# Optimization experiments

Measured on AMD Instinct MI355X. Metric: run time of the kernel, lower is better.

Reference implementation:

```python
import jax, jax.numpy as jnp
import numpy as np

B, S, T, C, H = 16, 64, 4096, 512, 8
D = C // H
NEG = jnp.float32(-1e30)


def setup_inputs() -> dict:
    key = jax.random.key(0)
    ks = jax.random.split(key, 12)
    x = jax.random.normal(ks[0], (1, C, 1), dtype=jnp.float32)
    eh = jax.random.normal(ks[1], (B, C, T), dtype=jnp.float32)
    # ragged shot boundaries -> fixed (B, S) start/end arrays, end > start
    bounds = jnp.sort(jax.random.randint(ks[2], (B, S + 1), 0, T), axis=-1)
    shot_starts = bounds[:, :-1].astype(jnp.int32)
    shot_ends = jnp.maximum(bounds[:, 1:], shot_starts + 1).astype(jnp.int32)
    sc = 1.0 / np.sqrt(C)
    Wq = jax.random.normal(ks[3], (C, C), dtype=jnp.float32) * sc
    bq = jnp.zeros((C,), dtype=jnp.float32)
    Wk = jax.random.normal(ks[4], (C, C), dtype=jnp.float32) * sc
    bk = jnp.zeros((C,), dtype=jnp.float32)
    Wv = jax.random.normal(ks[5], (C, C), dtype=jnp.float32) * sc
    bv = jnp.zeros((C,), dtype=jnp.float32)
    Wp = jax.random.normal(ks[6], (C, C), dtype=jnp.float32) * sc
    bp = jnp.zeros((C,), dtype=jnp.float32)
    return {"x": x, "encoder_hidden_states": eh, "shot_starts": shot_starts,
            "shot_ends": shot_ends, "Wq": Wq, "bq": bq, "Wk": Wk, "bk": bk,
            "Wv": Wv, "bv": bv, "Wp": Wp, "bp": bp}


def reference(x, encoder_hidden_states, shot_starts, shot_ends,
              Wq, bq, Wk, bk, Wv, bv, Wp, bp):
    scale = 1.0 / np.sqrt(D)
    # 1x1 conv == pointwise matmul over channels
    q = (Wq @ x[0] + bq[:, None])            # (C, 1)
    k = jnp.einsum('oc,bct->bot', Wk, encoder_hidden_states) + bk[None, :, None]
    v = jnp.einsum('oc,bct->bot', Wv, encoder_hidden_states) + bv[None, :, None]
    qh = q.reshape(H, D) * scale             # (H, D) single query per head
    kh = k.reshape(B, H, D, T)               # (B, H, D, T)
    vh = v.reshape(B, H, D, T).transpose(0, 1, 3, 2)  # (B, H, T, D)
    att = jnp.einsum('hd,bhdt->bht', qh, kh)          # (B, H, T)
    pos = jnp.arange(T)
    seg = (pos[None, None, :] >= shot_starts[:, :, None]) & \
          (pos[None, None, :] < shot_ends[:, :, None])  # (B, S, T)
    logits = jnp.where(seg[:, :, None, :], att[:, None, :, :], NEG)  # (B,S,H,T)
    p = jax.nn.softmax(logits, axis=-1)
    out = jnp.einsum('bsht,bhtd->bshd', p, vh)        # (B, S, H, D)
    out = out.reshape(B * S, C)
    out = out @ Wp.T + bp                              # proj (1x1 conv)
    return out[:, :, None]                             # (B*S, C, 1)
```

## Files before the change

kernel.cpp:

```cpp
#include <hip/hip_runtime.h>
#include <cstdint>
#include <cstddef>

#define B_ 16
#define S_ 64
#define T_ 4096
#define C_ 512
#define H_ 8

#define WS_QKT     0
#define WS_QB      4096
#define WS_QH      4104
#define WS_MS      4616
#define WS_LI      12808
#define WS_CNT     21000
#define WS_CSEG    21016
#define WS_CIDX    23064
#define WS_CMUL    25112
#define WS_ATT     28672
#define WS_WSUM    552960
#define WS_ATTNOUT 4747264

__global__ void k_prep1(const float* __restrict__ x, const float* __restrict__ Wq,
                        const float* __restrict__ bq, float* __restrict__ qh_g) {
  __shared__ float xs[C_];
  __shared__ float red[256];
  int tid = threadIdx.x;
  xs[tid] = x[tid];
  xs[tid + 256] = x[tid + 256];
  __syncthreads();
  int r0 = blockIdx.x * 32;
  int rl = tid >> 3, sub = tid & 7;
  int r = r0 + rl;
  const float* wr = Wq + (size_t)r * C_ + sub * 64;
  const float* xp = xs + sub * 64;
  float s = 0.f;
#pragma unroll
  for (int i = 0; i < 64; i += 4) {
    float4 w = *(const float4*)(wr + i);
    s += w.x * xp[i] + w.y * xp[i + 1] + w.z * xp[i + 2] + w.w * xp[i + 3];
  }
  red[tid] = s;
  __syncthreads();
  if (sub == 0) {
    float tot = bq[r];
#pragma unroll
    for (int i = 0; i < 8; ++i) tot += red[rl * 8 + i];
    qh_g[r] = tot * 0.125f;
  }
}

__global__ void k_prep2(const float* __restrict__ qh_g,
                        const float* __restrict__ Wk,
                        const float* __restrict__ bk, float* __restrict__ qkT,
                        float* __restrict__ qb) {
  __shared__ float qhs[64];
  int tid = threadIdx.x;
  int h = blockIdx.x;
  if (tid < 64) qhs[tid] = qh_g[h * 64 + tid];
  __syncthreads();
  int c0 = tid, c1 = tid + 256;
  float s0 = 0.f, s1 = 0.f;
#pragma unroll 8
  for (int d = 0; d < 64; ++d) {
    const float* row = Wk + (size_t)(h * 64 + d) * C_;
    float q = qhs[d];
    s0 += q * row[c0];
    s1 += q * row[c1];
  }
  qkT[c0 * 8 + h] = s0;
  qkT[c1 * 8 + h] = s1;
  if (tid < 64) {
    float w = qhs[tid] * bk[h * 64 + tid];
#pragma unroll
    for (int off = 32; off > 0; off >>= 1) w += __shfl_down(w, off, 64);
    if (tid == 0) qb[h] = w;
  }
}

__global__ __launch_bounds__(256, 4) void k_att(
    const float* __restrict__ eh, const float* __restrict__ qkT,
    const float* __restrict__ qb, float* __restrict__ att) {
  __shared__ float qks[C_ * 8];
  __shared__ float part[4 * 8 * 64];
  int tid = threadIdx.x;
  int tl = tid & 63, cg = tid >> 6;
  int b = blockIdx.y;
  int t0 = blockIdx.x * 64;
#pragma unroll
  for (int i = 0; i < 16; ++i) qks[tid + i * 256] = qkT[tid + i * 256];
  __syncthreads();
  const float* ehp = eh + ((size_t)b * C_ + (size_t)cg * 128) * T_ + t0 + tl;
  float acc[8];
#pragma unroll
  for (int h = 0; h < 8; ++h) acc[h] = 0.f;
#pragma unroll 4
  for (int j = 0; j < 128; ++j) {
    float e = ehp[(size_t)j * T_];
    const float4 q0 = *(const float4*)&qks[(cg * 128 + j) * 8];
    const float4 q1 = *(const float4*)&qks[(cg * 128 + j) * 8 + 4];
    acc[0] += q0.x * e; acc[1] += q0.y * e; acc[2] += q0.z * e; acc[3] += q0.w * e;
    acc[4] += q1.x * e; acc[5] += q1.y * e; acc[6] += q1.z * e; acc[7] += q1.w * e;
  }
#pragma unroll
  for (int h = 0; h < 8; ++h) part[(cg * 8 + h) * 64 + tl] = acc[h];
  __syncthreads();
#pragma unroll
  for (int i = 0; i < 2; ++i) {
    int idx = tid + i * 256;
    int h = idx >> 6, tt = idx & 63;
    float v = part[(0 * 8 + h) * 64 + tt] + part[(1 * 8 + h) * 64 + tt] +
              part[(2 * 8 + h) * 64 + tt] + part[(3 * 8 + h) * 64 + tt] + qb[h];
    att[((size_t)b * H_ + h) * T_ + t0 + tt] = v;
  }
}

__global__ void k_stats(const float* __restrict__ att,
                        const int* __restrict__ starts,
                        const int* __restrict__ ends, float* __restrict__ ms,
                        float* __restrict__ li) {
  int tid = threadIdx.x;
  int n = blockIdx.x;
  int b = n >> 6;
  int start = starts[n], end = ends[n];
  int h = tid >> 5, tl = tid & 31;
  const float* ah = att + ((size_t)b * H_ + h) * T_;
  float mloc = -3.0e38f;
  for (int t = start + tl; t < end; t += 32) mloc = fmaxf(mloc, ah[t]);
#pragma unroll
  for (int off = 16; off > 0; off >>= 1)
    mloc = fmaxf(mloc, __shfl_xor(mloc, off, 32));
  float lloc = 0.f;
  for (int t = start + tl; t < end; t += 32) lloc += __expf(ah[t] - mloc);
#pragma unroll
  for (int off = 16; off > 0; off >>= 1) lloc += __shfl_xor(lloc, off, 32);
  if (tl == 0) { ms[n * 8 + h] = mloc; li[n * 8 + h] = 1.f / lloc; }
}

__global__ void k_map(const int* __restrict__ starts,
                      const int* __restrict__ ends, int* __restrict__ cnt,
                      int* __restrict__ cseg, int* __restrict__ cidx,
                      int* __restrict__ cmul) {
  __shared__ int sc[1024];
  int n = threadIdx.x;
  int st = starts[n], en = ends[n];
  int cbase = st & ~15;
  int nch = (en - cbase + 127) >> 7;
  sc[n] = nch;
  __syncthreads();
  for (int off = 1; off < 1024; off <<= 1) {
    int v = 0;
    if (n >= off) v = sc[n - off];
    __syncthreads();
    sc[n] += v;
    __syncthreads();
  }
  int pre = sc[n] - nch;
  for (int k = 0; k < nch; ++k) {
    cseg[pre + k] = n;
    cidx[pre + k] = k;
    cmul[pre + k] = (nch > 1) ? 1 : 0;
  }
  if (n == 1023) cnt[0] = sc[n];
}

__global__ __launch_bounds__(256, 4) void k_wsum(
    const float* __restrict__ eh, const float* __restrict__ att,
    const float* __restrict__ ms, const float* __restrict__ li,
    const int* __restrict__ starts, const int* __restrict__ ends,
    const int* __restrict__ cnt, const int* __restrict__ cseg,
    const int* __restrict__ cidx, const int* __restrict__ cmul,
    float* __restrict__ wsum) {
  __shared__ float pl[8 * 136];
  int i = blockIdx.x;
  if (i >= cnt[0]) return;
  int tid = threadIdx.x;
  int n = cseg[i];
  int k = cidx[i];
  int mul = cmul[i];
  int b = n >> 6;
  int st = starts[n], en = ends[n];
  int cbase = st & ~15;
  int base = cbase + (k << 7);
  int t_lo = (st > base) ? st : base;
  int t_hi = base + 128;
  if (en < t_hi) t_hi = en;
  int jmax = t_hi - base;
  int kmax = (jmax + 15) >> 4;

  {
    int h = tid >> 5, l32 = tid & 31;
    float msn = ms[n * 8 + h], lin = li[n * 8 + h];
    const float* ah = att + ((size_t)b * H_ + h) * T_;
    for (int j = l32; j < 136; j += 32) {
      int t = base + j;
      float pv = 0.f;
      if (t >= t_lo && t < t_hi) pv = __expf(ah[t] - msn) * lin;
      pl[h * 136 + j] = pv;
    }
  }
  __syncthreads();

  int l = tid & 63, wv = tid >> 6;
  int il = l & 3, g = l >> 2;
  float* wp = wsum + (size_t)n * (H_ * C_);

  for (int pass = 0; pass < 8; ++pass) {
    int ch = pass * 64 + wv * 16 + g;
    const float* erow = eh + ((size_t)b * C_ + ch) * T_;
    float a0 = 0.f, a1 = 0.f, a2 = 0.f, a3 = 0.f;
    float a4 = 0.f, a5 = 0.f, a6 = 0.f, a7 = 0.f;
#pragma unroll 2
    for (int kk = 0; kk < kmax; ++kk) {
      int j0 = (kk << 4) | (il << 2);
      int tg = base + j0;
      if (tg > T_ - 4) tg = T_ - 4;
      float4 ev = *(const float4*)(erow + tg);
      const float* pp = pl + j0;
      float4 p;
      p = *(const float4*)(pp + 0 * 136);
      a0 += p.x * ev.x + p.y * ev.y + p.z * ev.z + p.w * ev.w;
      p = *(const float4*)(pp + 1 * 136);
      a1 += p.x * ev.x + p.y * ev.y + p.z * ev.z + p.w * ev.w;
      p = *(const float4*)(pp + 2 * 136);
      a2 += p.x * ev.x + p.y * ev.y + p.z * ev.z + p.w * ev.w;
      p = *(const float4*)(pp + 3 * 136);
      a3 += p.x * ev.x + p.y * ev.y + p.z * ev.z + p.w * ev.w;
      p = *(const float4*)(pp + 4 * 136);
      a4 += p.x * ev.x + p.y * ev.y + p.z * ev.z + p.w * ev.w;
      p = *(const float4*)(pp + 5 * 136);
      a5 += p.x * ev.x + p.y * ev.y + p.z * ev.z + p.w * ev.w;
      p = *(const float4*)(pp + 6 * 136);
      a6 += p.x * ev.x + p.y * ev.y + p.z * ev.z + p.w * ev.w;
      p = *(const float4*)(pp + 7 * 136);
      a7 += p.x * ev.x + p.y * ev.y + p.z * ev.z + p.w * ev.w;
    }
    a0 += __shfl_xor(a0, 1); a0 += __shfl_xor(a0, 2);
    a1 += __shfl_xor(a1, 1); a1 += __shfl_xor(a1, 2);
    a2 += __shfl_xor(a2, 1); a2 += __shfl_xor(a2, 2);
    a3 += __shfl_xor(a3, 1); a3 += __shfl_xor(a3, 2);
    a4 += __shfl_xor(a4, 1); a4 += __shfl_xor(a4, 2);
    a5 += __shfl_xor(a5, 1); a5 += __shfl_xor(a5, 2);
    a6 += __shfl_xor(a6, 1); a6 += __shfl_xor(a6, 2);
    a7 += __shfl_xor(a7, 1); a7 += __shfl_xor(a7, 2);
    float s0 = (il < 2) ? ((il == 0) ? a0 : a2) : ((il == 2) ? a4 : a6);
    float s1 = (il < 2) ? ((il == 0) ? a1 : a3) : ((il == 2) ? a5 : a7);
    int h0 = il << 1;
    if (!mul) {
      wp[h0 * C_ + ch] = s0;
      wp[(h0 + 1) * C_ + ch] = s1;
    } else {
      atomicAdd(&wp[h0 * C_ + ch], s0);
      atomicAdd(&wp[(h0 + 1) * C_ + ch], s1);
    }
  }
}

__global__ __launch_bounds__(256, 4) void k_gemm(
    const float* __restrict__ A, long aRow, long aColPerY,
    const float* __restrict__ Bm, const float* __restrict__ bias,
    float* __restrict__ Cc) {
  __shared__ float As[32 * 36];
  __shared__ float Bs[64 * 36];
  int tid = threadIdx.x;
  int n0 = blockIdx.x * 32;
  int y = blockIdx.y;
  const float* Abase = A + (size_t)n0 * aRow + (size_t)y * aColPerY;
  const float* Bbase = Bm + (size_t)(y * 64) * C_;
  int tx = tid & 15, ty = tid >> 4;
  float acc[2][4];
#pragma unroll
  for (int a = 0; a < 2; ++a)
#pragma unroll
    for (int bb = 0; bb < 4; ++bb) acc[a][bb] = 0.f;
  for (int k0 = 0; k0 < 512; k0 += 32) {
#pragma unroll
    for (int i = 0; i < 4; ++i) {
      int idx = tid + i * 256;
      int r = idx >> 5, cc = idx & 31;
      As[r * 36 + cc] = Abase[(size_t)r * aRow + k0 + cc];
    }
#pragma unroll
    for (int i = 0; i < 8; ++i) {
      int idx = tid + i * 256;
      int r = idx >> 5, cc = idx & 31;
      Bs[r * 36 + cc] = Bbase[(size_t)r * C_ + k0 + cc];
    }
    __syncthreads();
#pragma unroll
    for (int k = 0; k < 32; k += 4) {
      const float4 a0 = *(const float4*)&As[(ty * 2 + 0) * 36 + k];
      const float4 a1 = *(const float4*)&As[(ty * 2 + 1) * 36 + k];
#pragma unroll
      for (int bb = 0; bb < 4; ++bb) {
        const float4 bv = *(const float4*)&Bs[(tx * 4 + bb) * 36 + k];
        acc[0][bb] += a0.x * bv.x + a0.y * bv.y + a0.z * bv.z + a0.w * bv.w;
        acc[1][bb] += a1.x * bv.x + a1.y * bv.y + a1.z * bv.z + a1.w * bv.w;
      }
    }
    __syncthreads();
  }
#pragma unroll
  for (int a = 0; a < 2; ++a) {
    int nn = n0 + ty * 2 + a;
    float4 o;
    o.x = acc[a][0] + bias[y * 64 + tx * 4 + 0];
    o.y = acc[a][1] + bias[y * 64 + tx * 4 + 1];
    o.z = acc[a][2] + bias[y * 64 + tx * 4 + 2];
    o.w = acc[a][3] + bias[y * 64 + tx * 4 + 3];
    *(float4*)&Cc[(size_t)nn * C_ + y * 64 + tx * 4] = o;
  }
}

extern "C" void kernel_launch(void* const* d_in, const int* in_sizes, int n_in,
                              void* d_out, int out_size, void* d_ws,
                              size_t ws_size, hipStream_t stream) {
  const float* x = (const float*)d_in[0];
  const float* eh = (const float*)d_in[1];
  const int* shot_starts = (const int*)d_in[2];
  const int* shot_ends = (const int*)d_in[3];
  const float* Wq = (const float*)d_in[4];
  const float* bq = (const float*)d_in[5];
  const float* Wk = (const float*)d_in[6];
  const float* bk = (const float*)d_in[7];
  const float* Wv = (const float*)d_in[8];
  const float* bv = (const float*)d_in[9];
  const float* Wp = (const float*)d_in[10];
  const float* bp = (const float*)d_in[11];
  float* out = (float*)d_out;

  float* ws = (float*)d_ws;
  float* qkT = ws + WS_QKT;
  float* qb = ws + WS_QB;
  float* qh = ws + WS_QH;
  float* ms = ws + WS_MS;
  float* li = ws + WS_LI;
  int* cnt = (int*)(ws + WS_CNT);
  int* cseg = (int*)(ws + WS_CSEG);
  int* cidx = (int*)(ws + WS_CIDX);
  int* cmul = (int*)(ws + WS_CMUL);
  float* att = ws + WS_ATT;
  float* wsum = ws + WS_WSUM;
  float* attnout = ws + WS_ATTNOUT;

  hipMemsetAsync(wsum, 0, (size_t)1024 * H_ * C_ * sizeof(float), stream);
  k_prep1<<<16, 256, 0, stream>>>(x, Wq, bq, qh);
  k_prep2<<<8, 256, 0, stream>>>(qh, Wk, bk, qkT, qb);
  k_att<<<dim3(T_ / 64, B_), 256, 0, stream>>>(eh, qkT, qb, att);
  k_stats<<<B_ * S_, 256, 0, stream>>>(att, shot_starts, shot_ends, ms, li);
  k_map<<<1, 1024, 0, stream>>>(shot_starts, shot_ends, cnt, cseg, cidx, cmul);
  k_wsum<<<2048, 256, 0, stream>>>(eh, att, ms, li, shot_starts, shot_ends,
                                   cnt, cseg, cidx, cmul, wsum);
  k_gemm<<<dim3(32, 8), 256, 0, stream>>>(wsum, (long)(H_ * C_), (long)C_, Wv,
                                          bv, attnout);
  k_gemm<<<dim3(32, 8), 256, 0, stream>>>(attnout, (long)C_, 0L, Wp, bp, out);
}
```

Baseline: 347.4 us.

## Fold chunk mapping into stats kernel and block wsum over four channels

Removes the single-block k_map prefix-scan kernel: the chunk count is zeroed in k_prep1, and each k_stats block claims its chunk-list slots with an atomicAdd. This saves one launch and a serial 1024-thread scan. The order of chunks now depends on scheduling but stays consistent, and writes are clamped to 2048 entries. Separately, k_wsum now computes four channels per thread per pass instead of one, so each LDS probability load is reused across four eh rows, at the cost of 32 accumulators and more register pressure.

```diff
diff --git a/kernel.cpp b/kernel.cpp
--- a/kernel.cpp
+++ b/kernel.cpp
@@ -22,10 +22,12 @@
 #define WS_ATTNOUT 4747264
 
 __global__ void k_prep1(const float* __restrict__ x, const float* __restrict__ Wq,
-                        const float* __restrict__ bq, float* __restrict__ qh_g) {
+                        const float* __restrict__ bq, float* __restrict__ qh_g,
+                        int* __restrict__ cnt) {
   __shared__ float xs[C_];
   __shared__ float red[256];
   int tid = threadIdx.x;
+  if (blockIdx.x == 0 && tid == 0) cnt[0] = 0;
   xs[tid] = x[tid];
   xs[tid + 256] = x[tid + 256];
   __syncthreads();
@@ -118,11 +120,25 @@
 __global__ void k_stats(const float* __restrict__ att,
                         const int* __restrict__ starts,
                         const int* __restrict__ ends, float* __restrict__ ms,
-                        float* __restrict__ li) {
+                        float* __restrict__ li, int* __restrict__ cnt,
+                        int* __restrict__ cseg, int* __restrict__ cidx,
+                        int* __restrict__ cmul) {
   int tid = threadIdx.x;
   int n = blockIdx.x;
   int b = n >> 6;
   int start = starts[n], end = ends[n];
+  if (tid == 0) {
+    int cb = start & ~15;
+    int nch = (end - cb + 127) >> 7;
+    int pre = atomicAdd(cnt, nch);
+    int lim = 2048 - pre;
+    if (nch < lim) lim = nch;
+    for (int k = 0; k < lim; ++k) {
+      cseg[pre + k] = n;
+      cidx[pre + k] = k;
+      cmul[pre + k] = (nch > 1) ? 1 : 0;
+    }
+  }
   int h = tid >> 5, tl = tid & 31;
   const float* ah = att + ((size_t)b * H_ + h) * T_;
   float mloc = -3.0e38f;
@@ -135,33 +151,6 @@
 #pragma unroll
   for (int off = 16; off > 0; off >>= 1) lloc += __shfl_xor(lloc, off, 32);
   if (tl == 0) { ms[n * 8 + h] = mloc; li[n * 8 + h] = 1.f / lloc; }
-}
-
-__global__ void k_map(const int* __restrict__ starts,
-                      const int* __restrict__ ends, int* __restrict__ cnt,
-                      int* __restrict__ cseg, int* __restrict__ cidx,
-                      int* __restrict__ cmul) {
-  __shared__ int sc[1024];
-  int n = threadIdx.x;
-  int st = starts[n], en = ends[n];
-  int cbase = st & ~15;
-  int nch = (en - cbase + 127) >> 7;
-  sc[n] = nch;
-  __syncthreads();
-  for (int off = 1; off < 1024; off <<= 1) {
-    int v = 0;
-    if (n >= off) v = sc[n - off];
-    __syncthreads();
-    sc[n] += v;
-    __syncthreads();
-  }
-  int pre = sc[n] - nch;
-  for (int k = 0; k < nch; ++k) {
-    cseg[pre + k] = n;
-    cidx[pre + k] = k;
-    cmul[pre + k] = (nch > 1) ? 1 : 0;
-  }
-  if (n == 1023) cnt[0] = sc[n];
 }
 
 __global__ __launch_bounds__(256, 4) void k_wsum(
@@ -205,53 +194,58 @@
   int il = l & 3, g = l >> 2;
   float* wp = wsum + (size_t)n * (H_ * C_);
 
-  for (int pass = 0; pass < 8; ++pass) {
-    int ch = pass * 64 + wv * 16 + g;
-    const float* erow = eh + ((size_t)b * C_ + ch) * T_;
-    float a0 = 0.f, a1 = 0.f, a2 = 0.f, a3 = 0.f;
-    float a4 = 0.f, a5 = 0.f, a6 = 0.f, a7 = 0.f;
+#pragma unroll
+  for (int p2 = 0; p2 < 2; ++p2) {
+    int ch0 = p2 * 256 + wv * 64 + g;
+    const float* er0 = eh + ((size_t)b * C_ + ch0) * T_;
+    float acc[4][8];
+#pragma unroll
+    for (int cc = 0; cc < 4; ++cc)
+#pragma unroll
+      for (int h = 0; h < 8; ++h) acc[cc][h] = 0.f;
 #pragma unroll 2
     for (int kk = 0; kk < kmax; ++kk) {
       int j0 = (kk << 4) | (il << 2);
       int tg = base + j0;
       if (tg > T_ - 4) tg = T_ - 4;
-      float4 ev = *(const float4*)(erow + tg);
+      float4 ev[4];
+#pragma unroll
+      for (int cc = 0; cc < 4; ++cc)
+        ev[cc] = *(const float4*)(er0 + (size_t)(cc * 16) * T_ + tg);
       const float* pp = pl + j0;
-      float4 p;
-      p = *(const float4*)(pp + 0 * 136);
-      a0 += p.x * ev.x + p.y * ev.y + p.z * ev.z + p.w * ev.w;
-      p = *(const float4*)(pp + 1 * 136);
-      a1 += p.x * ev.x + p.y * ev.y + p.z * ev.z + p.w * ev.w;
-      p = *(const float4*)(pp + 2 * 136);
-      a2 += p.x * ev.x + p.y * ev.y + p.z * ev.z + p.w * ev.w;
-      p = *(const float4*)(pp + 3 * 136);
-      a3 += p.x * ev.x + p.y * ev.y + p.z * ev.z + p.w * ev.w;
-      p = *(const float4*)(pp + 4 * 136);
-      a4 += p.x * ev.x + p.y * ev.y + p.z * ev.z + p.w * ev.w;
-      p = *(const float4*)(pp + 5 * 136);
-      a5 += p.x * ev.x + p.y * ev.y + p.z * ev.z + p.w * ev.w;
-      p = *(const float4*)(pp + 6 * 136);
-      a6 += p.x * ev.x + p.y * ev.y + p.z * ev.z + p.w * ev.w;
-      p = *(const float4*)(pp + 7 * 136);
-      a7 += p.x * ev.x + p.y * ev.y + p.z * ev.z + p.w * ev.w;
-    }
-    a0 += __shfl_xor(a0, 1); a0 += __shfl_xor(a0, 2);
-    a1 += __shfl_xor(a1, 1); a1 += __shfl_xor(a1, 2);
-    a2 += __shfl_xor(a2, 1); a2 += __shfl_xor(a2, 2);
-    a3 += __shfl_xor(a3, 1); a3 += __shfl_xor(a3, 2);
-    a4 += __shfl_xor(a4, 1); a4 += __shfl_xor(a4, 2);
-    a5 += __shfl_xor(a5, 1); a5 += __shfl_xor(a5, 2);
-    a6 += __shfl_xor(a6, 1); a6 += __shfl_xor(a6, 2);
-    a7 += __shfl_xor(a7, 1); a7 += __shfl_xor(a7, 2);
-    float s0 = (il < 2) ? ((il == 0) ? a0 : a2) : ((il == 2) ? a4 : a6);
-    float s1 = (il < 2) ? ((il == 0) ? a1 : a3) : ((il == 2) ? a5 : a7);
-    int h0 = il << 1;
-    if (!mul) {
-      wp[h0 * C_ + ch] = s0;
-      wp[(h0 + 1) * C_ + ch] = s1;
-    } else {
-      atomicAdd(&wp[h0 * C_ + ch], s0);
-      atomicAdd(&wp[(h0 + 1) * C_ + ch], s1);
+#pragma unroll
+      for (int h = 0; h < 8; ++h) {
+        float4 pf = *(const float4*)(pp + h * 136);
+#pragma unroll
+        for (int cc = 0; cc < 4; ++cc)
+          acc[cc][h] += pf.x * ev[cc].x + pf.y * ev[cc].y +
+                        pf.z * ev[cc].z + pf.w * ev[cc].w;
+      }
+    }
+#pragma unroll
+    for (int cc = 0; cc < 4; ++cc)
+#pragma unroll
+      for (int h = 0; h < 8; ++h) {
+        acc[cc][h] += __shfl_xor(acc[cc][h], 1);
+        acc[cc][h] += __shfl_xor(acc[cc][h], 2);
+      }
+#pragma unroll
+    for (int cc = 0; cc < 4; ++cc) {
+      int ch = ch0 + cc * 16;
+      float s0 = (il == 0) ? acc[cc][0]
+               : (il == 1) ? acc[cc][2]
+               : (il == 2) ? acc[cc][4] : acc[cc][6];
+      float s1 = (il == 0) ? acc[cc][1]
+               : (il == 1) ? acc[cc][3]
+               : (il == 2) ? acc[cc][5] : acc[cc][7];
+      int h0 = il << 1;
+      if (!mul) {
+        wp[h0 * C_ + ch] = s0;
+        wp[(h0 + 1) * C_ + ch] = s1;
+      } else {
+        atomicAdd(&wp[h0 * C_ + ch], s0);
+        atomicAdd(&wp[(h0 + 1) * C_ + ch], s1);
+      }
     }
   }
 }
@@ -344,11 +338,11 @@
   float* attnout = ws + WS_ATTNOUT;
 
   hipMemsetAsync(wsum, 0, (size_t)1024 * H_ * C_ * sizeof(float), stream);
-  k_prep1<<<16, 256, 0, stream>>>(x, Wq, bq, qh);
+  k_prep1<<<16, 256, 0, stream>>>(x, Wq, bq, qh, cnt);
   k_prep2<<<8, 256, 0, stream>>>(qh, Wk, bk, qkT, qb);
   k_att<<<dim3(T_ / 64, B_), 256, 0, stream>>>(eh, qkT, qb, att);
-  k_stats<<<B_ * S_, 256, 0, stream>>>(att, shot_starts, shot_ends, ms, li);
-  k_map<<<1, 1024, 0, stream>>>(shot_starts, shot_ends, cnt, cseg, cidx, cmul);
+  k_stats<<<B_ * S_, 256, 0, stream>>>(att, shot_starts, shot_ends, ms, li,
+                                       cnt, cseg, cidx, cmul);
   k_wsum<<<2048, 256, 0, stream>>>(eh, att, ms, li, shot_starts, shot_ends,
                                    cnt, cseg, cidx, cmul, wsum);
   k_gemm<<<dim3(32, 8), 256, 0, stream>>>(wsum, (long)(H_ * C_), (long)C_, Wv,
```

After: 357.6 us. 2.9% more time.

## Fold chunk map into prep kernel, zero wsum selectively, widen attention tiles

Applied to the files above, without the earlier changes.

Moves the shot-chunk prefix-scan map into an extra block of k_prep1, which removes a separate single-block launch. The full memset of the wsum buffer is replaced by zeroing inside k_stats, and only for segments that span more than one chunk and so accumulate atomically. k_att now has each thread handle four timesteps with float4 loads, giving 256 timesteps per block and a quarter as many blocks. The trade-offs are a larger shared-memory buffer in k_att, fewer blocks to fill the GPU, and a correctness dependence on single-chunk segments writing every element of their wsum rows.

```diff
diff --git a/kernel.cpp b/kernel.cpp
--- a/kernel.cpp
+++ b/kernel.cpp
@@ -22,10 +22,51 @@
 #define WS_ATTNOUT 4747264
 
 __global__ void k_prep1(const float* __restrict__ x, const float* __restrict__ Wq,
-                        const float* __restrict__ bq, float* __restrict__ qh_g) {
+                        const float* __restrict__ bq, float* __restrict__ qh_g,
+                        const int* __restrict__ starts,
+                        const int* __restrict__ ends, int* __restrict__ cnt,
+                        int* __restrict__ cseg, int* __restrict__ cidx,
+                        int* __restrict__ cmul) {
   __shared__ float xs[C_];
   __shared__ float red[256];
-  int tid = threadIdx.x;
+  __shared__ int sc2[256];
+  int tid = threadIdx.x;
+  if (blockIdx.x == 16) {
+    int n0 = tid * 4;
+    int st0 = starts[n0 + 0], en0 = ends[n0 + 0];
+    int st1 = starts[n0 + 1], en1 = ends[n0 + 1];
+    int st2 = starts[n0 + 2], en2 = ends[n0 + 2];
+    int st3 = starts[n0 + 3], en3 = ends[n0 + 3];
+    int c0 = (en0 - (st0 & ~15) + 127) >> 7;
+    int c1 = (en1 - (st1 & ~15) + 127) >> 7;
+    int c2 = (en2 - (st2 & ~15) + 127) >> 7;
+    int c3 = (en3 - (st3 & ~15) + 127) >> 7;
+    int loc = c0 + c1 + c2 + c3;
+    sc2[tid] = loc;
+    __syncthreads();
+    for (int off = 1; off < 256; off <<= 1) {
+      int v = (tid >= off) ? sc2[tid - off] : 0;
+      __syncthreads();
+      sc2[tid] += v;
+      __syncthreads();
+    }
+    int pre = sc2[tid] - loc;
+#define EMIT(cX, nX)                                                  \
+    {                                                                 \
+      int m = (cX > 1) ? 1 : 0;                                       \
+      for (int k = 0; k < cX; ++k) {                                  \
+        cseg[pre + k] = nX; cidx[pre + k] = k; cmul[pre + k] = m;     \
+      }                                                               \
+      pre += cX;                                                      \
+    }
+    EMIT(c0, n0 + 0)
+    EMIT(c1, n0 + 1)
+    EMIT(c2, n0 + 2)
+    EMIT(c3, n0 + 3)
+#undef EMIT
+    if (tid == 255) cnt[0] = sc2[255];
+    return;
+  }
   xs[tid] = x[tid];
   xs[tid + 256] = x[tid + 256];
   __syncthreads();
@@ -82,35 +123,41 @@
     const float* __restrict__ eh, const float* __restrict__ qkT,
     const float* __restrict__ qb, float* __restrict__ att) {
   __shared__ float qks[C_ * 8];
-  __shared__ float part[4 * 8 * 64];
+  __shared__ float part[4 * 8 * 256];
   int tid = threadIdx.x;
   int tl = tid & 63, cg = tid >> 6;
   int b = blockIdx.y;
-  int t0 = blockIdx.x * 64;
+  int t0 = blockIdx.x * 256;
 #pragma unroll
   for (int i = 0; i < 16; ++i) qks[tid + i * 256] = qkT[tid + i * 256];
   __syncthreads();
-  const float* ehp = eh + ((size_t)b * C_ + (size_t)cg * 128) * T_ + t0 + tl;
-  float acc[8];
-#pragma unroll
-  for (int h = 0; h < 8; ++h) acc[h] = 0.f;
+  const float* ehp =
+      eh + ((size_t)b * C_ + (size_t)cg * 128) * T_ + t0 + tl * 4;
+  float4 acc[8];
+#pragma unroll
+  for (int h = 0; h < 8; ++h) acc[h] = make_float4(0.f, 0.f, 0.f, 0.f);
+#define FMA4(A, s)                                                       \
+  A.x += (s)*ev.x; A.y += (s)*ev.y; A.z += (s)*ev.z; A.w += (s)*ev.w;
 #pragma unroll 4
   for (int j = 0; j < 128; ++j) {
-    float e = ehp[(size_t)j * T_];
+    float4 ev = *(const float4*)&ehp[(size_t)j * T_];
     const float4 q0 = *(const float4*)&qks[(cg * 128 + j) * 8];
     const float4 q1 = *(const float4*)&qks[(cg * 128 + j) * 8 + 4];
-    acc[0] += q0.x * e; acc[1] += q0.y * e; acc[2] += q0.z * e; acc[3] += q0.w * e;
-    acc[4] += q1.x * e; acc[5] += q1.y * e; acc[6] += q1.z * e; acc[7] += q1.w * e;
-  }
-#pragma unroll
-  for (int h = 0; h < 8; ++h) part[(cg * 8 + h) * 64 + tl] = acc[h];
-  __syncthreads();
-#pragma unroll
-  for (int i = 0; i < 2; ++i) {
+    FMA4(acc[0], q0.x) FMA4(acc[1], q0.y) FMA4(acc[2], q0.z) FMA4(acc[3], q0.w)
+    FMA4(acc[4], q1.x) FMA4(acc[5], q1.y) FMA4(acc[6], q1.z) FMA4(acc[7], q1.w)
+  }
+#undef FMA4
+#pragma unroll
+  for (int h = 0; h < 8; ++h)
+    *(float4*)&part[(cg * 8 + h) * 256 + tl * 4] = acc[h];
+  __syncthreads();
+#pragma unroll
+  for (int i = 0; i < 8; ++i) {
     int idx = tid + i * 256;
-    int h = idx >> 6, tt = idx & 63;
-    float v = part[(0 * 8 + h) * 64 + tt] + part[(1 * 8 + h) * 64 + tt] +
-              part[(2 * 8 + h) * 64 + tt] + part[(3 * 8 + h) * 64 + tt] + qb[h];
+    int h = idx >> 8, tt = idx & 255;
+    float v = part[(0 * 8 + h) * 256 + tt] + part[(1 * 8 + h) * 256 + tt] +
+              part[(2 * 8 + h) * 256 + tt] + part[(3 * 8 + h) * 256 + tt] +
+              qb[h];
     att[((size_t)b * H_ + h) * T_ + t0 + tt] = v;
   }
 }
@@ -118,11 +165,18 @@
 __global__ void k_stats(const float* __restrict__ att,
                         const int* __restrict__ starts,
                         const int* __restrict__ ends, float* __restrict__ ms,
-                        float* __restrict__ li) {
+                        float* __restrict__ li, float* __restrict__ wsum) {
   int tid = threadIdx.x;
   int n = blockIdx.x;
   int b = n >> 6;
   int start = starts[n], end = ends[n];
+  int nch = (end - (start & ~15) + 127) >> 7;
+  if (nch > 1) {
+    float4 z = make_float4(0.f, 0.f, 0.f, 0.f);
+    float* wrow = wsum + (size_t)n * (H_ * C_);
+#pragma unroll
+    for (int i2 = 0; i2 < 4; ++i2) *(float4*)&wrow[(tid + i2 * 256) * 4] = z;
+  }
   int h = tid >> 5, tl = tid & 31;
   const float* ah = att + ((size_t)b * H_ + h) * T_;
   float mloc = -3.0e38f;
@@ -135,33 +189,6 @@
 #pragma unroll
   for (int off = 16; off > 0; off >>= 1) lloc += __shfl_xor(lloc, off, 32);
   if (tl == 0) { ms[n * 8 + h] = mloc; li[n * 8 + h] = 1.f / lloc; }
-}
-
-__global__ void k_map(const int* __restrict__ starts,
-                      const int* __restrict__ ends, int* __restrict__ cnt,
-                      int* __restrict__ cseg, int* __restrict__ cidx,
-                      int* __restrict__ cmul) {
-  __shared__ int sc[1024];
-  int n = threadIdx.x;
-  int st = starts[n], en = ends[n];
-  int cbase = st & ~15;
-  int nch = (en - cbase + 127) >> 7;
-  sc[n] = nch;
-  __syncthreads();
-  for (int off = 1; off < 1024; off <<= 1) {
-    int v = 0;
-    if (n >= off) v = sc[n - off];
-    __syncthreads();
-    sc[n] += v;
-    __syncthreads();
-  }
-  int pre = sc[n] - nch;
-  for (int k = 0; k < nch; ++k) {
-    cseg[pre + k] = n;
-    cidx[pre + k] = k;
-    cmul[pre + k] = (nch > 1) ? 1 : 0;
-  }
-  if (n == 1023) cnt[0] = sc[n];
 }
 
 __global__ __launch_bounds__(256, 4) void k_wsum(
@@ -343,12 +370,12 @@
   float* wsum = ws + WS_WSUM;
   float* attnout = ws + WS_ATTNOUT;
 
-  hipMemsetAsync(wsum, 0, (size_t)1024 * H_ * C_ * sizeof(float), stream);
-  k_prep1<<<16, 256, 0, stream>>>(x, Wq, bq, qh);
+  k_prep1<<<17, 256, 0, stream>>>(x, Wq, bq, qh, shot_starts, shot_ends, cnt,
+                                  cseg, cidx, cmul);
   k_prep2<<<8, 256, 0, stream>>>(qh, Wk, bk, qkT, qb);
-  k_att<<<dim3(T_ / 64, B_), 256, 0, stream>>>(eh, qkT, qb, att);
-  k_stats<<<B_ * S_, 256, 0, stream>>>(att, shot_starts, shot_ends, ms, li);
-  k_map<<<1, 1024, 0, stream>>>(shot_starts, shot_ends, cnt, cseg, cidx, cmul);
+  k_att<<<dim3(T_ / 256, B_), 256, 0, stream>>>(eh, qkT, qb, att);
+  k_stats<<<B_ * S_, 256, 0, stream>>>(att, shot_starts, shot_ends, ms, li,
+                                       wsum);
   k_wsum<<<2048, 256, 0, stream>>>(eh, att, ms, li, shot_starts, shot_ends,
                                    cnt, cseg, cidx, cmul, wsum);
   k_gemm<<<dim3(32, 8), 256, 0, stream>>>(wsum, (long)(H_ * C_), (long)C_, Wv,
```

Measured after the change: 339.1 us, median of 2. -2.4%, faster.

## Fuse attention logits, segment softmax, and weighted sum into one per-segment kernel

Applied to the files above, without the earlier changes.

Replaces the separate logit, stats, chunk-map and weighted-sum kernels with one kernel that runs one block per shot segment. Each block walks its segment in 64-token chunks: it recomputes the logits from the encoder states, applies an online softmax with running max and sum in shared memory, and accumulates the weighted channel sums in shared memory. This removes the global logit buffer round trip, the memset, the atomics and several launches. The cost is that one block processes a whole segment serially, so long segments cause load imbalance, and the larger shared-memory footprint lowers the occupancy target.

```diff
diff --git a/kernel.cpp b/kernel.cpp
--- a/kernel.cpp
+++ b/kernel.cpp
@@ -11,13 +11,6 @@
 #define WS_QKT     0
 #define WS_QB      4096
 #define WS_QH      4104
-#define WS_MS      4616
-#define WS_LI      12808
-#define WS_CNT     21000
-#define WS_CSEG    21016
-#define WS_CIDX    23064
-#define WS_CMUL    25112
-#define WS_ATT     28672
 #define WS_WSUM    552960
 #define WS_ATTNOUT 4747264
 
@@ -78,181 +71,171 @@
   }
 }
 
-__global__ __launch_bounds__(256, 4) void k_att(
+__global__ __launch_bounds__(256, 3) void k_fused(
     const float* __restrict__ eh, const float* __restrict__ qkT,
-    const float* __restrict__ qb, float* __restrict__ att) {
-  __shared__ float qks[C_ * 8];
-  __shared__ float part[4 * 8 * 64];
-  int tid = threadIdx.x;
-  int tl = tid & 63, cg = tid >> 6;
-  int b = blockIdx.y;
-  int t0 = blockIdx.x * 64;
-#pragma unroll
-  for (int i = 0; i < 16; ++i) qks[tid + i * 256] = qkT[tid + i * 256];
-  __syncthreads();
-  const float* ehp = eh + ((size_t)b * C_ + (size_t)cg * 128) * T_ + t0 + tl;
-  float acc[8];
-#pragma unroll
-  for (int h = 0; h < 8; ++h) acc[h] = 0.f;
-#pragma unroll 4
-  for (int j = 0; j < 128; ++j) {
-    float e = ehp[(size_t)j * T_];
-    const float4 q0 = *(const float4*)&qks[(cg * 128 + j) * 8];
-    const float4 q1 = *(const float4*)&qks[(cg * 128 + j) * 8 + 4];
-    acc[0] += q0.x * e; acc[1] += q0.y * e; acc[2] += q0.z * e; acc[3] += q0.w * e;
-    acc[4] += q1.x * e; acc[5] += q1.y * e; acc[6] += q1.z * e; acc[7] += q1.w * e;
-  }
-#pragma unroll
-  for (int h = 0; h < 8; ++h) part[(cg * 8 + h) * 64 + tl] = acc[h];
-  __syncthreads();
-#pragma unroll
-  for (int i = 0; i < 2; ++i) {
-    int idx = tid + i * 256;
-    int h = idx >> 6, tt = idx & 63;
-    float v = part[(0 * 8 + h) * 64 + tt] + part[(1 * 8 + h) * 64 + tt] +
-              part[(2 * 8 + h) * 64 + tt] + part[(3 * 8 + h) * 64 + tt] + qb[h];
-    att[((size_t)b * H_ + h) * T_ + t0 + tt] = v;
-  }
-}
-
-__global__ void k_stats(const float* __restrict__ att,
-                        const int* __restrict__ starts,
-                        const int* __restrict__ ends, float* __restrict__ ms,
-                        float* __restrict__ li) {
+    const float* __restrict__ qb_g, const int* __restrict__ starts,
+    const int* __restrict__ ends, float* __restrict__ wsum) {
+  __shared__ __attribute__((aligned(16))) float qks[C_ * 8];
+  __shared__ __attribute__((aligned(16))) float part[4 * 8 * 64];
+  __shared__ __attribute__((aligned(16))) float ps[8 * 72];
+  __shared__ __attribute__((aligned(16))) float accw[C_ * 8];
+  __shared__ float qbs[8], mlds[8], llds[8], flds[8];
   int tid = threadIdx.x;
   int n = blockIdx.x;
   int b = n >> 6;
-  int start = starts[n], end = ends[n];
-  int h = tid >> 5, tl = tid & 31;
-  const float* ah = att + ((size_t)b * H_ + h) * T_;
-  float mloc = -3.0e38f;
-  for (int t = start + tl; t < end; t += 32) mloc = fmaxf(mloc, ah[t]);
-#pragma unroll
-  for (int off = 16; off > 0; off >>= 1)
-    mloc = fmaxf(mloc, __shfl_xor(mloc, off, 32));
-  float lloc = 0.f;
-  for (int t = start + tl; t < end; t += 32) lloc += __expf(ah[t] - mloc);
-#pragma unroll
-  for (int off = 16; off > 0; off >>= 1) lloc += __shfl_xor(lloc, off, 32);
-  if (tl == 0) { ms[n * 8 + h] = mloc; li[n * 8 + h] = 1.f / lloc; }
-}
-
-__global__ void k_map(const int* __restrict__ starts,
-                      const int* __restrict__ ends, int* __restrict__ cnt,
-                      int* __restrict__ cseg, int* __restrict__ cidx,
-                      int* __restrict__ cmul) {
-  __shared__ int sc[1024];
-  int n = threadIdx.x;
   int st = starts[n], en = ends[n];
-  int cbase = st & ~15;
-  int nch = (en - cbase + 127) >> 7;
-  sc[n] = nch;
+  int base0 = st & ~15;
+  int nch = (en - base0 + 63) >> 6;
+
+#pragma unroll
+  for (int i2 = 0; i2 < 16; ++i2) qks[tid + i2 * 256] = qkT[tid + i2 * 256];
+#pragma unroll
+  for (int i2 = 0; i2 < 16; ++i2) accw[tid + i2 * 256] = 0.f;
+  if (tid < 8) {
+    qbs[tid] = qb_g[tid];
+    mlds[tid] = -3.0e38f;
+    llds[tid] = 0.f;
+  }
   __syncthreads();
-  for (int off = 1; off < 1024; off <<= 1) {
-    int v = 0;
-    if (n >= off) v = sc[n - off];
-    __syncthreads();
-    sc[n] += v;
-    __syncthreads();
-  }
-  int pre = sc[n] - nch;
-  for (int k = 0; k < nch; ++k) {
-    cseg[pre + k] = n;
-    cidx[pre + k] = k;
-    cmul[pre + k] = (nch > 1) ? 1 : 0;
-  }
-  if (n == 1023) cnt[0] = sc[n];
-}
-
-__global__ __launch_bounds__(256, 4) void k_wsum(
-    const float* __restrict__ eh, const float* __restrict__ att,
-    const float* __restrict__ ms, const float* __restrict__ li,
-    const int* __restrict__ starts, const int* __restrict__ ends,
-    const int* __restrict__ cnt, const int* __restrict__ cseg,
-    const int* __restrict__ cidx, const int* __restrict__ cmul,
-    float* __restrict__ wsum) {
-  __shared__ float pl[8 * 136];
-  int i = blockIdx.x;
-  if (i >= cnt[0]) return;
-  int tid = threadIdx.x;
-  int n = cseg[i];
-  int k = cidx[i];
-  int mul = cmul[i];
-  int b = n >> 6;
-  int st = starts[n], en = ends[n];
-  int cbase = st & ~15;
-  int base = cbase + (k << 7);
-  int t_lo = (st > base) ? st : base;
-  int t_hi = base + 128;
-  if (en < t_hi) t_hi = en;
-  int jmax = t_hi - base;
-  int kmax = (jmax + 15) >> 4;
-
-  {
-    int h = tid >> 5, l32 = tid & 31;
-    float msn = ms[n * 8 + h], lin = li[n * 8 + h];
-    const float* ah = att + ((size_t)b * H_ + h) * T_;
-    for (int j = l32; j < 136; j += 32) {
-      int t = base + j;
-      float pv = 0.f;
-      if (t >= t_lo && t < t_hi) pv = __expf(ah[t] - msn) * lin;
-      pl[h * 136 + j] = pv;
-    }
-  }
-  __syncthreads();
-
-  int l = tid & 63, wv = tid >> 6;
-  int il = l & 3, g = l >> 2;
+
+  int tl = tid & 63, cg = tid >> 6;
+  int il = tl & 3, g = tl >> 2, wv = cg;
+  int hh = tid >> 5, l32 = tid & 31;
+
+  for (int c = 0; c < nch; ++c) {
+    int t0 = base0 + (c << 6);
+
+    {
+      int tt = t0 + tl;
+      if (tt > T_ - 1) tt = T_ - 1;
+      const float* ehp = eh + ((size_t)b * C_ + (size_t)cg * 128) * T_ + tt;
+      float a0 = 0.f, a1 = 0.f, a2 = 0.f, a3 = 0.f;
+      float a4 = 0.f, a5 = 0.f, a6 = 0.f, a7 = 0.f;
+#pragma unroll 4
+      for (int j = 0; j < 128; ++j) {
+        float e = ehp[(size_t)j * T_];
+        const float4 q0 = *(const float4*)&qks[(cg * 128 + j) * 8];
+        const float4 q1 = *(const float4*)&qks[(cg * 128 + j) * 8 + 4];
+        a0 += q0.x * e; a1 += q0.y * e; a2 += q0.z * e; a3 += q0.w * e;
+        a4 += q1.x * e; a5 += q1.y * e; a6 += q1.z * e; a7 += q1.w * e;
+      }
+      part[(cg * 8 + 0) * 64 + tl] = a0;
+      part[(cg * 8 + 1) * 64 + tl] = a1;
+      part[(cg * 8 + 2) * 64 + tl] = a2;
+      part[(cg * 8 + 3) * 64 + tl] = a3;
+      part[(cg * 8 + 4) * 64 + tl] = a4;
+      part[(cg * 8 + 5) * 64 + tl] = a5;
+      part[(cg * 8 + 6) * 64 + tl] = a6;
+      part[(cg * 8 + 7) * 64 + tl] = a7;
+    }
+    __syncthreads();
+#pragma unroll
+    for (int i2 = 0; i2 < 2; ++i2) {
+      int idx = tid + i2 * 256;
+      int h = idx >> 6, tt2 = idx & 63;
+      int t = t0 + tt2;
+      float v = part[(0 * 8 + h) * 64 + tt2] + part[(1 * 8 + h) * 64 + tt2] +
+                part[(2 * 8 + h) * 64 + tt2] + part[(3 * 8 + h) * 64 + tt2] +
+                qbs[h];
+      ps[h * 72 + tt2] = (t >= st && t < en) ? v : -3.0e38f;
+    }
+    __syncthreads();
+
+    {
+      float v0 = ps[hh * 72 + l32], v1 = ps[hh * 72 + 32 + l32];
+      float cmax = fmaxf(v0, v1);
+#pragma unroll
+      for (int off = 16; off > 0; off >>= 1)
+        cmax = fmaxf(cmax, __shfl_xor(cmax, off, 32));
+      float mo = mlds[hh];
+      float mn = fmaxf(mo, cmax);
+      float f = __expf(mo - mn);
+      float p0 = __expf(v0 - mn), p1 = __expf(v1 - mn);
+      ps[hh * 72 + l32] = p0;
+      ps[hh * 72 + 32 + l32] = p1;
+      float cs = p0 + p1;
+#pragma unroll
+      for (int off = 16; off > 0; off >>= 1) cs += __shfl_xor(cs, off, 32);
+      if (l32 == 0) {
+        mlds[hh] = mn;
+        llds[hh] = llds[hh] * f + cs;
+        flds[hh] = f;
+      }
+    }
+    __syncthreads();
+
+    {
+      float f0 = flds[0], f1 = flds[1], f2 = flds[2], f3 = flds[3];
+      float f4 = flds[4], f5 = flds[5], f6 = flds[6], f7 = flds[7];
+      int base4 = tid * 16;
+      float4 w0 = *(float4*)&accw[base4 + 0];
+      float4 w1 = *(float4*)&accw[base4 + 4];
+      float4 w2 = *(float4*)&accw[base4 + 8];
+      float4 w3 = *(float4*)&accw[base4 + 12];
+      w0.x *= f0; w0.y *= f1; w0.z *= f2; w0.w *= f3;
+      w1.x *= f4; w1.y *= f5; w1.z *= f6; w1.w *= f7;
+      w2.x *= f0; w2.y *= f1; w2.z *= f2; w2.w *= f3;
+      w3.x *= f4; w3.y *= f5; w3.z *= f6; w3.w *= f7;
+      *(float4*)&accw[base4 + 0] = w0;
+      *(float4*)&accw[base4 + 4] = w1;
+      *(float4*)&accw[base4 + 8] = w2;
+      *(float4*)&accw[base4 + 12] = w3;
+    }
+    __syncthreads();
+#pragma unroll
+    for (int pass = 0; pass < 8; ++pass) {
+      int ch = pass * 64 + wv * 16 + g;
+      const float* erow = eh + ((size_t)b * C_ + ch) * T_;
+      float a0 = 0.f, a1 = 0.f, a2 = 0.f, a3 = 0.f;
+      float a4 = 0.f, a5 = 0.f, a6 = 0.f, a7 = 0.f;
+#pragma unroll
+      for (int kk = 0; kk < 4; ++kk) {
+        int j0 = (kk << 4) | (il << 2);
+        int tg = t0 + j0;
+        if (tg > T_ - 4) tg = T_ - 4;
+        float4 ev = *(const float4*)(erow + tg);
+        const float* pp = ps + j0;
+        float4 p;
+        p = *(const float4*)(pp + 0 * 72);
+        a0 += p.x * ev.x + p.y * ev.y + p.z * ev.z + p.w * ev.w;
+        p = *(const float4*)(pp + 1 * 72);
+        a1 += p.x * ev.x + p.y * ev.y + p.z * ev.z + p.w * ev.w;
+        p = *(const float4*)(pp + 2 * 72);
+        a2 += p.x * ev.x + p.y * ev.y + p.z * ev.z + p.w * ev.w;
+        p = *(const float4*)(pp + 3 * 72);
+        a3 += p.x * ev.x + p.y * ev.y + p.z * ev.z + p.w * ev.w;
+        p = *(const float4*)(pp + 4 * 72);
+        a4 += p.x * ev.x + p.y * ev.y + p.z * ev.z + p.w * ev.w;
+        p = *(const float4*)(pp + 5 * 72);
+        a5 += p.x * ev.x + p.y * ev.y + p.z * ev.z + p.w * ev.w;
+        p = *(const float4*)(pp + 6 * 72);
+        a6 += p.x * ev.x + p.y * ev.y + p.z * ev.z + p.w * ev.w;
+        p = *(const float4*)(pp + 7 * 72);
+        a7 += p.x * ev.x + p.y * ev.y + p.z * ev.z + p.w * ev.w;
+      }
+      a0 += __shfl_xor(a0, 1); a0 += __shfl_xor(a0, 2);
+      a1 += __shfl_xor(a1, 1); a1 += __shfl_xor(a1, 2);
+      a2 += __shfl_xor(a2, 1); a2 += __shfl_xor(a2, 2);
+      a3 += __shfl_xor(a3, 1); a3 += __shfl_xor(a3, 2);
+      a4 += __shfl_xor(a4, 1); a4 += __shfl_xor(a4, 2);
+      a5 += __shfl_xor(a5, 1); a5 += __shfl_xor(a5, 2);
+      a6 += __shfl_xor(a6, 1); a6 += __shfl_xor(a6, 2);
+      a7 += __shfl_xor(a7, 1); a7 += __shfl_xor(a7, 2);
+      float s0 = (il < 2) ? ((il == 0) ? a0 : a2) : ((il == 2) ? a4 : a6);
+      float s1 = (il < 2) ? ((il == 0) ? a1 : a3) : ((il == 2) ? a5 : a7);
+      int h0 = il << 1;
+      accw[ch * 8 + h0] += s0;
+      accw[ch * 8 + h0 + 1] += s1;
+    }
+    __syncthreads();
+  }
+
   float* wp = wsum + (size_t)n * (H_ * C_);
-
-  for (int pass = 0; pass < 8; ++pass) {
-    int ch = pass * 64 + wv * 16 + g;
-    const float* erow = eh + ((size_t)b * C_ + ch) * T_;
-    float a0 = 0.f, a1 = 0.f, a2 = 0.f, a3 = 0.f;
-    float a4 = 0.f, a5 = 0.f, a6 = 0.f, a7 = 0.f;
-#pragma unroll 2
-    for (int kk = 0; kk < kmax; ++kk) {
-      int j0 = (kk << 4) | (il << 2);
-      int tg = base + j0;
-      if (tg > T_ - 4) tg = T_ - 4;
-      float4 ev = *(const float4*)(erow + tg);
-      const float* pp = pl + j0;
-      float4 p;
-      p = *(const float4*)(pp + 0 * 136);
-      a0 += p.x * ev.x + p.y * ev.y + p.z * ev.z + p.w * ev.w;
-      p = *(const float4*)(pp + 1 * 136);
-      a1 += p.x * ev.x + p.y * ev.y + p.z * ev.z + p.w * ev.w;
-      p = *(const float4*)(pp + 2 * 136);
-      a2 += p.x * ev.x + p.y * ev.y + p.z * ev.z + p.w * ev.w;
-      p = *(const float4*)(pp + 3 * 136);
-      a3 += p.x * ev.x + p.y * ev.y + p.z * ev.z + p.w * ev.w;
-      p = *(const float4*)(pp + 4 * 136);
-      a4 += p.x * ev.x + p.y * ev.y + p.z * ev.z + p.w * ev.w;
-      p = *(const float4*)(pp + 5 * 136);
-      a5 += p.x * ev.x + p.y * ev.y + p.z * ev.z + p.w * ev.w;
-      p = *(const float4*)(pp + 6 * 136);
-      a6 += p.x * ev.x + p.y * ev.y + p.z * ev.z + p.w * ev.w;
-      p = *(const float4*)(pp + 7 * 136);
-      a7 += p.x * ev.x + p.y * ev.y + p.z * ev.z + p.w * ev.w;
-    }
-    a0 += __shfl_xor(a0, 1); a0 += __shfl_xor(a0, 2);
-    a1 += __shfl_xor(a1, 1); a1 += __shfl_xor(a1, 2);
-    a2 += __shfl_xor(a2, 1); a2 += __shfl_xor(a2, 2);
-    a3 += __shfl_xor(a3, 1); a3 += __shfl_xor(a3, 2);
-    a4 += __shfl_xor(a4, 1); a4 += __shfl_xor(a4, 2);
-    a5 += __shfl_xor(a5, 1); a5 += __shfl_xor(a5, 2);
-    a6 += __shfl_xor(a6, 1); a6 += __shfl_xor(a6, 2);
-    a7 += __shfl_xor(a7, 1); a7 += __shfl_xor(a7, 2);
-    float s0 = (il < 2) ? ((il == 0) ? a0 : a2) : ((il == 2) ? a4 : a6);
-    float s1 = (il < 2) ? ((il == 0) ? a1 : a3) : ((il == 2) ? a5 : a7);
-    int h0 = il << 1;
-    if (!mul) {
-      wp[h0 * C_ + ch] = s0;
-      wp[(h0 + 1) * C_ + ch] = s1;
-    } else {
-      atomicAdd(&wp[h0 * C_ + ch], s0);
-      atomicAdd(&wp[(h0 + 1) * C_ + ch], s1);
-    }
+#pragma unroll
+  for (int h = 0; h < 8; ++h) {
+    float inv = 1.f / llds[h];
+    wp[h * C_ + tid] = accw[tid * 8 + h] * inv;
+    wp[h * C_ + 256 + tid] = accw[(256 + tid) * 8 + h] * inv;
   }
 }
 
@@ -333,24 +316,13 @@
   float* qkT = ws + WS_QKT;
   float* qb = ws + WS_QB;
   float* qh = ws + WS_QH;
-  float* ms = ws + WS_MS;
-  float* li = ws + WS_LI;
-  int* cnt = (int*)(ws + WS_CNT);
-  int* cseg = (int*)(ws + WS_CSEG);
-  int* cidx = (int*)(ws + WS_CIDX);
-  int* cmul = (int*)(ws + WS_CMUL);
-  float* att = ws + WS_ATT;
   float* wsum = ws + WS_WSUM;
   float* attnout = ws + WS_ATTNOUT;
 
-  hipMemsetAsync(wsum, 0, (size_t)1024 * H_ * C_ * sizeof(float), stream);
   k_prep1<<<16, 256, 0, stream>>>(x, Wq, bq, qh);
   k_prep2<<<8, 256, 0, stream>>>(qh, Wk, bk, qkT, qb);
-  k_att<<<dim3(T_ / 64, B_), 256, 0, stream>>>(eh, qkT, qb, att);
-  k_stats<<<B_ * S_, 256, 0, stream>>>(att, shot_starts, shot_ends, ms, li);
-  k_map<<<1, 1024, 0, stream>>>(shot_starts, shot_ends, cnt, cseg, cidx, cmul);
-  k_wsum<<<2048, 256, 0, stream>>>(eh, att, ms, li, shot_starts, shot_ends,
-                                   cnt, cseg, cidx, cmul, wsum);
+  k_fused<<<B_ * S_, 256, 0, stream>>>(eh, qkT, qb, shot_starts, shot_ends,
+                                       wsum);
   k_gemm<<<dim3(32, 8), 256, 0, stream>>>(wsum, (long)(H_ * C_), (long)C_, Wv,
                                           bv, attnout);
   k_gemm<<<dim3(32, 8), 256, 0, stream>>>(attnout, (long)C_, 0L, Wp, bp, out);
```

Measured after the change: 603.2 us. +73.6%, slower.
